# Kernel tuning notes

Hardware: AMD Instinct MI355X
Metric: run time of the kernel (lower is better)

The kernel has to match this reference:

```python
import jax, jax.numpy as jnp
import numpy as np

N = 50000   # nodes
E = 800000  # edges
D = 128     # input feature dim
H = 128     # hidden_channels
O = 128     # out_channels
NEG_SLOPE = 0.2


def setup_inputs() -> dict:
    key = jax.random.key(0)
    ks = jax.random.split(key, 16)
    x = jax.random.normal(ks[0], (N, D), dtype=jnp.float32)
    edge_idx = jax.random.randint(ks[1], (2, E), 0, N, dtype=jnp.int32)

    def lin(k, fin, fout):
        return jax.random.normal(k, (fin, fout), dtype=jnp.float32) / np.sqrt(fin)

    params = {
        # layer 1 (D -> H)
        "Wl1": lin(ks[2], D, H), "bl1": jnp.zeros((H,), jnp.float32),
        "Wr1": lin(ks[3], D, H), "br1": jnp.zeros((H,), jnp.float32),
        "att1": jax.random.normal(ks[4], (H,), dtype=jnp.float32) / np.sqrt(H),
        "b1": jnp.zeros((H,), jnp.float32),
        # layer 2 (H -> O)
        "Wl2": lin(ks[5], H, O), "bl2": jnp.zeros((O,), jnp.float32),
        "Wr2": lin(ks[6], H, O), "br2": jnp.zeros((O,), jnp.float32),
        "att2": jax.random.normal(ks[7], (O,), dtype=jnp.float32) / np.sqrt(O),
        "b2": jnp.zeros((O,), jnp.float32),
    }
    return {"x": x, "edge_idx": edge_idx, **params}


def gatv2_layer(x, src, dst, Wl, bl, Wr, br, att, bias):
    """Single-head GATv2Conv (add_self_loops=False), PyG semantics.

    message(x_j) uses lin_l(x_j); score uses leaky_relu(lin_l(x_j)+lin_r(x_i)) @ att,
    softmax over in-edges of each target node, scatter-add weighted messages.
    """
    xl = x @ Wl + bl            # [N, F] source transform
    xr = x @ Wr + br            # [N, F] target transform
    msg = xl[src]               # [E, F] gathered source messages
    e = jax.nn.leaky_relu(msg + xr[dst], NEG_SLOPE)  # [E, F]
    s = e @ att                 # [E] unnormalized scores
    smax = jax.lax.stop_gradient(jax.ops.segment_max(s, dst, num_segments=N))
    p = jnp.exp(s - smax[dst])  # stable segment softmax numerator
    denom = jax.ops.segment_sum(p, dst, num_segments=N)  # [N]
    alpha = p / denom[dst]      # [E]
    out = jax.ops.segment_sum(alpha[:, None] * msg, dst, num_segments=N)
    return out + bias


def reference(x, edge_idx, Wl1, bl1, Wr1, br1, att1, b1, Wl2, bl2, Wr2, br2, att2, b2):
    src, dst = edge_idx[0], edge_idx[1]
    h = jax.nn.relu(gatv2_layer(x, src, dst, Wl1, bl1, Wr1, br1, att1, b1))
    out = gatv2_layer(h, src, dst, Wl2, bl2, Wr2, br2, att2, b2)
    return out
```

## Files before the change

### kernel.cpp

```cpp
#include <hip/hip_runtime.h>
#include <math.h>


typedef short bf16x8 __attribute__((ext_vector_type(8)));
typedef float f32x4 __attribute__((ext_vector_type(4)));

#define LDK 136

__global__ __launch_bounds__(256) void prep_zero_kernel(
    const float* __restrict__ W0, const float* __restrict__ W1,
    const float* __restrict__ W2, const float* __restrict__ W3,
    short* __restrict__ wt, int* __restrict__ deg8, int total8N) {
    int b = blockIdx.x;
    for (int j = b * 256 + threadIdx.x; j < total8N; j += 32 * 256) deg8[j] = 0;
    int mat = b >> 3, chunk = b & 7;
    const float* W = (mat == 0) ? W0 : (mat == 1) ? W1 : (mat == 2) ? W2 : W3;
    short* hi = wt + (size_t)mat * 2 * 16384;
    short* lo = hi + 16384;
    int i0 = chunk * 2048;
    for (int i = i0 + threadIdx.x; i < i0 + 2048; i += 256) {
        int k = i >> 7, n = i & 127;
        float x = W[i];
        unsigned u = __float_as_uint(x);
        unsigned hu = u & 0xFFFF0000u;
        float lf = x - __uint_as_float(hu);
        hi[n * 128 + k] = (short)(hu >> 16);
        lo[n * 128 + k] = (short)(__float_as_uint(lf) >> 16);
    }
}

__device__ __forceinline__ void gemm_dual32_body(
    int bx, const float* __restrict__ X, const short* __restrict__ wtL,
    const float* __restrict__ b0, short* __restrict__ out0bf,
    const float* __restrict__ b1, float* __restrict__ out1,
    int Nrows, short (&Ahi)[32][LDK], short (&Alo)[32][LDK]) {
    int tid = threadIdx.x;
    int w = tid >> 6, lane = tid & 63, q = lane >> 4, tr = lane & 15;
    int m0 = bx * 32;
    int n0 = w * 32;

    bf16x8 bh[4], bl[4];
    #pragma unroll
    for (int p = 0; p < 2; ++p) {
        const short* base = wtL + (size_t)p * 2 * 16384;
        #pragma unroll
        for (int nt = 0; nt < 2; ++nt) {
            size_t boff = (size_t)(n0 + nt * 16 + tr) * 128 + q * 8;
            bh[p * 2 + nt] = *(const bf16x8*)&base[boff];
            bl[p * 2 + nt] = *(const bf16x8*)&base[16384 + boff];
        }
    }

    {
        int srow = tid >> 3;
        int c0 = (tid & 7) * 16;
        int gr = m0 + srow; if (gr >= Nrows) gr = Nrows - 1;
        const float* xp = &X[(size_t)gr * 128 + c0];
        float4 v[4];
        #pragma unroll
        for (int j = 0; j < 4; ++j) v[j] = *(const float4*)(xp + j * 4);
        #pragma unroll
        for (int j = 0; j < 2; ++j) {
            bf16x8 hv, lv;
            #pragma unroll
            for (int k = 0; k < 2; ++k) {
                float4 vv = v[j * 2 + k];
                float f[4] = {vv.x, vv.y, vv.z, vv.w};
                #pragma unroll
                for (int e = 0; e < 4; ++e) {
                    unsigned u = __float_as_uint(f[e]);
                    unsigned hu = u & 0xFFFF0000u;
                    float lf = f[e] - __uint_as_float(hu);
                    hv[k * 4 + e] = (short)(hu >> 16);
                    lv[k * 4 + e] = (short)(__float_as_uint(lf) >> 16);
                }
            }
            *(bf16x8*)&Ahi[srow][c0 + j * 8] = hv;
            *(bf16x8*)&Alo[srow][c0 + j * 8] = lv;
        }
    }
    __syncthreads();

    f32x4 acc[2][4];
    #pragma unroll
    for (int a = 0; a < 2; ++a)
        #pragma unroll
        for (int b = 0; b < 4; ++b) acc[a][b] = (f32x4){0.f, 0.f, 0.f, 0.f};

    for (int kc = 0; kc < 128; kc += 32) {
        #pragma unroll
        for (int mt = 0; mt < 2; ++mt) {
            bf16x8 ah = *(const bf16x8*)&Ahi[mt * 16 + tr][kc + q * 8];
            bf16x8 al = *(const bf16x8*)&Alo[mt * 16 + tr][kc + q * 8];
            #pragma unroll
            for (int j = 0; j < 4; ++j) {
                acc[mt][j] = __builtin_amdgcn_mfma_f32_16x16x32_bf16(ah, bh[j], acc[mt][j], 0, 0, 0);
                acc[mt][j] = __builtin_amdgcn_mfma_f32_16x16x32_bf16(ah, bl[j], acc[mt][j], 0, 0, 0);
                acc[mt][j] = __builtin_amdgcn_mfma_f32_16x16x32_bf16(al, bh[j], acc[mt][j], 0, 0, 0);
            }
        }
        if (kc < 96) {
            #pragma unroll
            for (int p = 0; p < 2; ++p) {
                const short* base = wtL + (size_t)p * 2 * 16384;
                #pragma unroll
                for (int nt = 0; nt < 2; ++nt) {
                    size_t boff = (size_t)(n0 + nt * 16 + tr) * 128 + (kc + 32) + q * 8;
                    bh[p * 2 + nt] = *(const bf16x8*)&base[boff];
                    bl[p * 2 + nt] = *(const bf16x8*)&base[16384 + boff];
                }
            }
        }
    }

    #pragma unroll
    for (int nt = 0; nt < 2; ++nt) {
        float bv0 = b0[n0 + nt * 16 + tr];
        float bv1 = b1[n0 + nt * 16 + tr];
        #pragma unroll
        for (int mt = 0; mt < 2; ++mt) {
            #pragma unroll
            for (int r = 0; r < 4; ++r) {
                int row = m0 + mt * 16 + q * 4 + r;
                if (row < Nrows) {
                    float v0 = acc[mt][nt][r] + bv0;
                    unsigned u = __float_as_uint(v0);
                    unsigned rb = (u + 0x7FFFu + ((u >> 16) & 1u)) >> 16;
                    out0bf[(size_t)row * 128 + n0 + nt * 16 + tr] = (short)rb;
                    out1[(size_t)row * 128 + n0 + nt * 16 + tr] = acc[mt][2 + nt][r] + bv1;
                }
            }
        }
    }
}

__global__ __launch_bounds__(256) void gemm_mfma_dual32_kernel(
    const float* __restrict__ X, const short* __restrict__ wtL,
    const float* __restrict__ b0, short* __restrict__ out0bf,
    const float* __restrict__ b1, float* __restrict__ out1, int Nrows) {
    __shared__ __attribute__((aligned(16))) short Ahi[32][LDK];
    __shared__ __attribute__((aligned(16))) short Alo[32][LDK];
    gemm_dual32_body(blockIdx.x, X, wtL, b0, out0bf, b1, out1, Nrows, Ahi, Alo);
}

__global__ __launch_bounds__(256) void gemm1_count_kernel(
    const float* __restrict__ X, const short* __restrict__ wtL,
    const float* __restrict__ b0, short* __restrict__ out0bf,
    const float* __restrict__ b1, float* __restrict__ out1,
    int Nrows, int gemmBlocks,
    const int* __restrict__ dst, int* __restrict__ deg8,
    unsigned short* __restrict__ rank16, int E, int N) {
    __shared__ __attribute__((aligned(16))) short Ahi[32][LDK];
    __shared__ __attribute__((aligned(16))) short Alo[32][LDK];
    if ((int)blockIdx.x < gemmBlocks) {
        gemm_dual32_body(blockIdx.x, X, wtL, b0, out0bf, b1, out1, Nrows, Ahi, Alo);
    } else {
        int i = (blockIdx.x - gemmBlocks) * 256 + threadIdx.x;
        if (i < E) {
            int slice = (i >> 8) & 7;
            int r = atomicAdd(&deg8[(size_t)slice * N + dst[i]], 1);
            rank16[i] = (unsigned short)r;
        }
    }
}

__global__ __launch_bounds__(256) void scan_blocksum2_kernel(
    const int* __restrict__ deg8, unsigned short* __restrict__ base8,
    int* __restrict__ dtot, int* __restrict__ blockSums, int n) {
    __shared__ int wsum[4];
    int tid = threadIdx.x;
    int idx = blockIdx.x * 256 + tid;
    int lane = tid & 63, wid = tid >> 6;
    int tot = 0;
    if (idx < n) {
        int b = 0;
        #pragma unroll
        for (int s = 0; s < 8; ++s) {
            int v = deg8[(size_t)s * n + idx];
            base8[(size_t)s * n + idx] = (unsigned short)b;
            b += v;
        }
        tot = b;
        dtot[idx] = tot;
    }
    int v = tot;
    #pragma unroll
    for (int off = 32; off > 0; off >>= 1) v += __shfl_xor(v, off);
    if (lane == 0) wsum[wid] = v;
    __syncthreads();
    if (tid == 0) blockSums[blockIdx.x] = wsum[0] + wsum[1] + wsum[2] + wsum[3];
}

__global__ __launch_bounds__(256) void scan_apply2_kernel(
    const int* __restrict__ dtot, const int* __restrict__ blockSums,
    const unsigned short* __restrict__ base8,
    int* __restrict__ row_ptr, int* __restrict__ rpb, int n, int nBlk) {
    __shared__ int sPre[4], sAll[4], wsum[4];
    int tid = threadIdx.x, lane = tid & 63, wid = tid >> 6;

    int bsv = (tid < nBlk) ? blockSums[tid] : 0;
    int pre = (tid < (int)blockIdx.x) ? bsv : 0;
    int all = bsv;
    #pragma unroll
    for (int off = 32; off > 0; off >>= 1) {
        pre += __shfl_xor(pre, off);
        all += __shfl_xor(all, off);
    }
    if (lane == 0) { sPre[wid] = pre; sAll[wid] = all; }
    __syncthreads();
    int off0 = sPre[0] + sPre[1] + sPre[2] + sPre[3];
    int total = sAll[0] + sAll[1] + sAll[2] + sAll[3];

    int idx = blockIdx.x * 256 + tid;
    int v = (idx < n) ? dtot[idx] : 0;
    int incl = v;
    #pragma unroll
    for (int off = 1; off < 64; off <<= 1) {
        int t = __shfl_up(incl, off);
        if (lane >= off) incl += t;
    }
    if (lane == 63) wsum[wid] = incl;
    __syncthreads();
    int woff = 0;
    #pragma unroll
    for (int w = 0; w < 4; ++w) woff += (w < wid) ? wsum[w] : 0;
    int excl = off0 + woff + (incl - v);
    if (idx < n) {
        row_ptr[idx] = excl;
        #pragma unroll
        for (int s = 0; s < 8; ++s)
            rpb[(size_t)s * n + idx] = excl + (int)base8[(size_t)s * n + idx];
    }
    if (blockIdx.x == 0 && tid == 0) row_ptr[n] = total;
}

__global__ void scatter_edges_kernel(const int* __restrict__ src, const int* __restrict__ dst,
                                     const int* __restrict__ rpb,
                                     const unsigned short* __restrict__ rank16,
                                     unsigned short* __restrict__ csr16, int E, int N) {
    int i = blockIdx.x * blockDim.x + threadIdx.x;
    if (i < E) {
        int d = dst[i];
        int slice = (i >> 8) & 7;
        int pos = rpb[(size_t)slice * N + d] + (int)rank16[i];
        csr16[pos] = (unsigned short)src[i];
    }
}

__global__ __launch_bounds__(256) void gat_aggregate_kernel(
    const short* __restrict__ xl16, const float* __restrict__ xr,
    const float* __restrict__ att, const float* __restrict__ bias,
    const int* __restrict__ row_ptr, const unsigned short* __restrict__ csr16,
    float* __restrict__ out, int N, int applyRelu) {
    int wid = threadIdx.x >> 6;
    int lane = threadIdx.x & 63;
    int qlane = lane & 15;
    int qid = lane >> 4;
    int node = blockIdx.x * 4 + wid;
    if (node >= N) return;

    const bf16x8* xlb = (const bf16x8*)xl16;
    float4 xrA = ((const float4*)xr)[(size_t)node * 32 + qlane * 2];
    float4 xrB = ((const float4*)xr)[(size_t)node * 32 + qlane * 2 + 1];
    float4 atA = ((const float4*)att)[qlane * 2];
    float4 atB = ((const float4*)att)[qlane * 2 + 1];

    int beg = row_ptr[node];
    int end = row_ptr[node + 1];

    float dsum = 0.f;
    float4 accA = {0.f, 0.f, 0.f, 0.f};
    float4 accB = {0.f, 0.f, 0.f, 0.f};

    for (int cbase = beg; cbase < end; cbase += 64) {
        int cnt = end - cbase;
        if (cnt > 64) cnt = 64;
        int myidx = (lane < cnt) ? (int)csr16[cbase + lane] : 0;
        int nq = (cnt + 3) >> 2;

        for (int g = 0; g < nq; ++g) {
            int eidx = 4 * g + qid;
            int s = __shfl(myidx, eidx);
            bf16x8 mv = xlb[((size_t)s << 4) + qlane];
            float4 vA, vB;
            vA.x = __uint_as_float(((unsigned)(unsigned short)mv[0]) << 16);
            vA.y = __uint_as_float(((unsigned)(unsigned short)mv[1]) << 16);
            vA.z = __uint_as_float(((unsigned)(unsigned short)mv[2]) << 16);
            vA.w = __uint_as_float(((unsigned)(unsigned short)mv[3]) << 16);
            vB.x = __uint_as_float(((unsigned)(unsigned short)mv[4]) << 16);
            vB.y = __uint_as_float(((unsigned)(unsigned short)mv[5]) << 16);
            vB.z = __uint_as_float(((unsigned)(unsigned short)mv[6]) << 16);
            vB.w = __uint_as_float(((unsigned)(unsigned short)mv[7]) << 16);

            float t, p;
            t = vA.x + xrA.x; t = fmaxf(t, 0.2f * t); p = t * atA.x;
            t = vA.y + xrA.y; t = fmaxf(t, 0.2f * t); p = fmaf(t, atA.y, p);
            t = vA.z + xrA.z; t = fmaxf(t, 0.2f * t); p = fmaf(t, atA.z, p);
            t = vA.w + xrA.w; t = fmaxf(t, 0.2f * t); p = fmaf(t, atA.w, p);
            t = vB.x + xrB.x; t = fmaxf(t, 0.2f * t); p = fmaf(t, atB.x, p);
            t = vB.y + xrB.y; t = fmaxf(t, 0.2f * t); p = fmaf(t, atB.y, p);
            t = vB.z + xrB.z; t = fmaxf(t, 0.2f * t); p = fmaf(t, atB.z, p);
            t = vB.w + xrB.w; t = fmaxf(t, 0.2f * t); p = fmaf(t, atB.w, p);

            p += __shfl_xor(p, 1);
            p += __shfl_xor(p, 2);
            p += __shfl_xor(p, 4);
            p += __shfl_xor(p, 8);

            float e = (eidx < cnt) ? __expf(p) : 0.f;
            dsum += e;
            accA.x = fmaf(e, vA.x, accA.x);
            accA.y = fmaf(e, vA.y, accA.y);
            accA.z = fmaf(e, vA.z, accA.z);
            accA.w = fmaf(e, vA.w, accA.w);
            accB.x = fmaf(e, vB.x, accB.x);
            accB.y = fmaf(e, vB.y, accB.y);
            accB.z = fmaf(e, vB.z, accB.z);
            accB.w = fmaf(e, vB.w, accB.w);
        }
    }

    #pragma unroll
    for (int off = 16; off <= 32; off <<= 1) {
        dsum += __shfl_xor(dsum, off);
        accA.x += __shfl_xor(accA.x, off);
        accA.y += __shfl_xor(accA.y, off);
        accA.z += __shfl_xor(accA.z, off);
        accA.w += __shfl_xor(accA.w, off);
        accB.x += __shfl_xor(accB.x, off);
        accB.y += __shfl_xor(accB.y, off);
        accB.z += __shfl_xor(accB.z, off);
        accB.w += __shfl_xor(accB.w, off);
    }

    float inv = dsum > 0.f ? 1.f / dsum : 0.f;
    float4 bvA = ((const float4*)bias)[qlane * 2];
    float4 bvB = ((const float4*)bias)[qlane * 2 + 1];
    float4 oA, oB;
    oA.x = accA.x * inv + bvA.x; oA.y = accA.y * inv + bvA.y;
    oA.z = accA.z * inv + bvA.z; oA.w = accA.w * inv + bvA.w;
    oB.x = accB.x * inv + bvB.x; oB.y = accB.y * inv + bvB.y;
    oB.z = accB.z * inv + bvB.z; oB.w = accB.w * inv + bvB.w;
    if (applyRelu) {
        oA.x = fmaxf(oA.x, 0.f); oA.y = fmaxf(oA.y, 0.f);
        oA.z = fmaxf(oA.z, 0.f); oA.w = fmaxf(oA.w, 0.f);
        oB.x = fmaxf(oB.x, 0.f); oB.y = fmaxf(oB.y, 0.f);
        oB.z = fmaxf(oB.z, 0.f); oB.w = fmaxf(oB.w, 0.f);
    }
    if (lane < 16) {
        ((float4*)out)[(size_t)node * 32 + qlane * 2] = oA;
        ((float4*)out)[(size_t)node * 32 + qlane * 2 + 1] = oB;
    }
}


extern "C" void kernel_launch(void* const* d_in, const int* in_sizes, int n_in,
                              void* d_out, int out_size, void* d_ws, size_t ws_size,
                              hipStream_t stream) {
    const float* x    = (const float*)d_in[0];
    const int* eidx   = (const int*)d_in[1];
    const float* Wl1  = (const float*)d_in[2];
    const float* bl1  = (const float*)d_in[3];
    const float* Wr1  = (const float*)d_in[4];
    const float* br1  = (const float*)d_in[5];
    const float* att1 = (const float*)d_in[6];
    const float* b1   = (const float*)d_in[7];
    const float* Wl2  = (const float*)d_in[8];
    const float* bl2  = (const float*)d_in[9];
    const float* Wr2  = (const float*)d_in[10];
    const float* br2  = (const float*)d_in[11];
    const float* att2 = (const float*)d_in[12];
    const float* b2   = (const float*)d_in[13];

    const int N = in_sizes[0] / 128;
    const int E = in_sizes[1] / 2;
    const int* src = eidx;
    const int* dst = eidx + E;

    const int nBlk = (N + 255) / 256;

    size_t NF = (size_t)N * 128;
    short* xl16 = (short*)d_ws;
    float* bufB = (float*)(xl16 + NF);
    float* bufC = bufB + NF;
    int* deg8      = (int*)(bufC + NF);
    int* dtot      = deg8 + 8 * (size_t)N;
    int* row_ptr   = dtot + N;
    int* blockSums = row_ptr + (N + 1);
    int* rpb       = blockSums + nBlk;
    unsigned short* base8  = (unsigned short*)(rpb + 8 * (size_t)N);
    unsigned short* rank16 = base8 + 8 * (size_t)N;
    unsigned short* csr16  = rank16 + E;
    short* wt      = (short*)(csr16 + E);

    float* outF = (float*)d_out;

    const int nCnt = (E + 255) / 256;
    const int gemmBlocks = (N + 31) / 32;
    dim3 aggGrid((N + 3) / 4);

    prep_zero_kernel<<<32, 256, 0, stream>>>(Wl1, Wr1, Wl2, Wr2, wt, deg8, 8 * N);
    gemm1_count_kernel<<<gemmBlocks + nCnt, 256, 0, stream>>>(
        x, wt, bl1, xl16, br1, bufB, N, gemmBlocks, dst, deg8, rank16, E, N);
    scan_blocksum2_kernel<<<nBlk, 256, 0, stream>>>(deg8, base8, dtot, blockSums, N);
    scan_apply2_kernel<<<nBlk, 256, 0, stream>>>(dtot, blockSums, base8, row_ptr, rpb, N, nBlk);
    scatter_edges_kernel<<<nCnt, 256, 0, stream>>>(src, dst, rpb, rank16, csr16, E, N);
    gat_aggregate_kernel<<<aggGrid, 256, 0, stream>>>(xl16, bufB, att1, b1, row_ptr, csr16,
                                                      bufC, N, 1);
    gemm_mfma_dual32_kernel<<<gemmBlocks, 256, 0, stream>>>(bufC, wt + 2 * 2 * 16384, bl2, xl16,
                                                            br2, bufB, N);
    gat_aggregate_kernel<<<aggGrid, 256, 0, stream>>>(xl16, bufB, att2, b2, row_ptr, csr16,
                                                      outF, N, 0);
}
```

Measured before the change: 294.3 us.

## Stage GEMM epilogue through LDS for vector stores and interleave count blocks

New measurement: 286.3 us. 1.03x faster.

```diff
diff --git a/kernel.cpp b/kernel.cpp
--- a/kernel.cpp
+++ b/kernel.cpp
@@ -6,6 +6,7 @@
 typedef float f32x4 __attribute__((ext_vector_type(4)));
 
 #define LDK 136
+#define SMEM_BYTES (2 * 32 * LDK * 2)
 
 __global__ __launch_bounds__(256) void prep_zero_kernel(
     const float* __restrict__ W0, const float* __restrict__ W1,
@@ -33,7 +34,10 @@
     int bx, const float* __restrict__ X, const short* __restrict__ wtL,
     const float* __restrict__ b0, short* __restrict__ out0bf,
     const float* __restrict__ b1, float* __restrict__ out1,
-    int Nrows, short (&Ahi)[32][LDK], short (&Alo)[32][LDK]) {
+    int Nrows, char* smem) {
+    short (*Ahi)[LDK] = (short (*)[LDK])smem;
+    short (*Alo)[LDK] = (short (*)[LDK])(smem + 32 * LDK * 2);
+
     int tid = threadIdx.x;
     int w = tid >> 6, lane = tid & 63, q = lane >> 4, tr = lane & 15;
     int m0 = bx * 32;
@@ -113,24 +117,47 @@
         }
     }
 
+    int orow = tid >> 3;
+    int oc0 = (tid & 7) * 16;
+    int gr = m0 + orow;
+
+    float (*Ofp)[132] = (float (*)[132])smem;
+    __syncthreads();
+    #pragma unroll
+    for (int nt = 0; nt < 2; ++nt) {
+        float bv1 = b1[n0 + nt * 16 + tr];
+        #pragma unroll
+        for (int mt = 0; mt < 2; ++mt)
+            #pragma unroll
+            for (int r = 0; r < 4; ++r)
+                Ofp[mt * 16 + q * 4 + r][n0 + nt * 16 + tr] = acc[mt][2 + nt][r] + bv1;
+    }
+    __syncthreads();
+    if (gr < Nrows) {
+        #pragma unroll
+        for (int j = 0; j < 4; ++j)
+            *(float4*)&out1[(size_t)gr * 128 + oc0 + j * 4] = *(float4*)&Ofp[orow][oc0 + j * 4];
+    }
+    __syncthreads();
+
+    short (*Obf)[136] = (short (*)[136])smem;
     #pragma unroll
     for (int nt = 0; nt < 2; ++nt) {
         float bv0 = b0[n0 + nt * 16 + tr];
-        float bv1 = b1[n0 + nt * 16 + tr];
-        #pragma unroll
-        for (int mt = 0; mt < 2; ++mt) {
+        #pragma unroll
+        for (int mt = 0; mt < 2; ++mt)
             #pragma unroll
             for (int r = 0; r < 4; ++r) {
-                int row = m0 + mt * 16 + q * 4 + r;
-                if (row < Nrows) {
-                    float v0 = acc[mt][nt][r] + bv0;
-                    unsigned u = __float_as_uint(v0);
-                    unsigned rb = (u + 0x7FFFu + ((u >> 16) & 1u)) >> 16;
-                    out0bf[(size_t)row * 128 + n0 + nt * 16 + tr] = (short)rb;
-                    out1[(size_t)row * 128 + n0 + nt * 16 + tr] = acc[mt][2 + nt][r] + bv1;
-                }
+                float v0 = acc[mt][nt][r] + bv0;
+                unsigned u = __float_as_uint(v0);
+                unsigned rb = (u + 0x7FFFu + ((u >> 16) & 1u)) >> 16;
+                Obf[mt * 16 + q * 4 + r][n0 + nt * 16 + tr] = (short)rb;
             }
-        }
+    }
+    __syncthreads();
+    if (gr < Nrows) {
+        *(bf16x8*)&out0bf[(size_t)gr * 128 + oc0]     = *(bf16x8*)&Obf[orow][oc0];
+        *(bf16x8*)&out0bf[(size_t)gr * 128 + oc0 + 8] = *(bf16x8*)&Obf[orow][oc0 + 8];
     }
 }
 
@@ -138,9 +165,8 @@
     const float* __restrict__ X, const short* __restrict__ wtL,
     const float* __restrict__ b0, short* __restrict__ out0bf,
     const float* __restrict__ b1, float* __restrict__ out1, int Nrows) {
-    __shared__ __attribute__((aligned(16))) short Ahi[32][LDK];
-    __shared__ __attribute__((aligned(16))) short Alo[32][LDK];
-    gemm_dual32_body(blockIdx.x, X, wtL, b0, out0bf, b1, out1, Nrows, Ahi, Alo);
+    __shared__ __attribute__((aligned(16))) char smem[SMEM_BYTES];
+    gemm_dual32_body(blockIdx.x, X, wtL, b0, out0bf, b1, out1, Nrows, smem);
 }
 
 __global__ __launch_bounds__(256) void gemm1_count_kernel(
@@ -150,17 +176,25 @@
     int Nrows, int gemmBlocks,
     const int* __restrict__ dst, int* __restrict__ deg8,
     unsigned short* __restrict__ rank16, int E, int N) {
-    __shared__ __attribute__((aligned(16))) short Ahi[32][LDK];
-    __shared__ __attribute__((aligned(16))) short Alo[32][LDK];
-    if ((int)blockIdx.x < gemmBlocks) {
-        gemm_dual32_body(blockIdx.x, X, wtL, b0, out0bf, b1, out1, Nrows, Ahi, Alo);
+    __shared__ __attribute__((aligned(16))) char smem[SMEM_BYTES];
+    int bx = blockIdx.x;
+    int base3 = 3 * gemmBlocks;
+    int cb;
+    if (bx < base3) {
+        int role = bx % 3, g = bx / 3;
+        if (role == 0) {
+            gemm_dual32_body(g, X, wtL, b0, out0bf, b1, out1, Nrows, smem);
+            return;
+        }
+        cb = g * 2 + (role - 1);
     } else {
-        int i = (blockIdx.x - gemmBlocks) * 256 + threadIdx.x;
-        if (i < E) {
-            int slice = (i >> 8) & 7;
-            int r = atomicAdd(&deg8[(size_t)slice * N + dst[i]], 1);
-            rank16[i] = (unsigned short)r;
-        }
+        cb = 2 * gemmBlocks + (bx - base3);
+    }
+    int i = cb * 256 + threadIdx.x;
+    if (i < E) {
+        int slice = (i >> 8) & 7;
+        int r = atomicAdd(&deg8[(size_t)slice * N + dst[i]], 1);
+        rank16[i] = (unsigned short)r;
     }
 }
 
@@ -397,10 +431,12 @@
 
     const int nCnt = (E + 255) / 256;
     const int gemmBlocks = (N + 31) / 32;
+    int fusedGrid = 3 * gemmBlocks;
+    if (nCnt > 2 * gemmBlocks) fusedGrid += nCnt - 2 * gemmBlocks;
     dim3 aggGrid((N + 3) / 4);
 
     prep_zero_kernel<<<32, 256, 0, stream>>>(Wl1, Wr1, Wl2, Wr2, wt, deg8, 8 * N);
-    gemm1_count_kernel<<<gemmBlocks + nCnt, 256, 0, stream>>>(
+    gemm1_count_kernel<<<fusedGrid, 256, 0, stream>>>(
         x, wt, bl1, xl16, br1, bufB, N, gemmBlocks, dst, deg8, rank16, E, N);
     scan_blocksum2_kernel<<<nBlk, 256, 0, stream>>>(deg8, base8, dtot, blockSums, N);
     scan_apply2_kernel<<<nBlk, 256, 0, stream>>>(dtot, blockSums, base8, row_ptr, rpb, N, nBlk);
```
